# Performance work log

Hardware: AMD Instinct MI355X
Metric: run time of the kernel (lower is better)

## Reference

```python
import jax, jax.numpy as jnp
import numpy as np

N, D = 512, 128


def setup_inputs() -> dict:
    key = jax.random.key(0)
    k1, k2 = jax.random.split(key)
    source = jax.random.normal(k1, (N, D), dtype=jnp.float32)
    target = jax.random.normal(k2, (N, D), dtype=jnp.float32)
    return {"source": source, "target": target}


def _distance_matrix(x):
    # pairwise squared-euclidean distances, same broadcast form as torch source
    return jnp.sum((x[:, None, :] - x[None, :, :]) ** 2, axis=-1)  # [n,n]


def reference(source, target):
    n = source.shape[0]
    C_s = _distance_matrix(source)  # [n,n]
    C_t = _distance_matrix(target)  # [n,n]
    # cost[i,j,k] = |C_s[i,j] - C_t[i,k]|  -> [n,n,n]
    cost = jnp.abs(C_s[:, :, None] - C_t[:, None, :])
    # transport_plan = outer(1/n, 1/n) is constant uniform 1/n^2;
    # the torch loop recomputes the identical value max_iter times, so one pass suffices.
    plan = jnp.float32(1.0) / (n * n)
    gw_dist = jnp.sum(cost * cost) * plan
    return gw_dist
```

## Files before the change

kernel.cpp:

```cpp
#include <hip/hip_runtime.h>

#define N 512
#define D 128


__device__ __forceinline__ float wave_reduce_add_f32(float v) {
    #pragma unroll
    for (int off = 32; off > 0; off >>= 1)
        v += __shfl_down(v, off, 64);
    return v;
}

__global__ __launch_bounds__(256) void gw_dist(
    const float* __restrict__ src, const float* __restrict__ tgt,
    double* __restrict__ rs, double* __restrict__ ss)
{
    __shared__ float tile[32 * 257];
    __shared__ float redf[4][8];

    const int b  = blockIdx.x;
    const int m  = b >> 8;
    const int iq = (b >> 1) & 127;
    const int jh = b & 1;
    const int t  = threadIdx.x;
    const int i0 = iq * 4;
    const int j0 = jh * 256;

    const float*  X  = m ? tgt : src;
    const float4* X4 = reinterpret_cast<const float4*>(X + j0 * D);

    const int jhome = t >> 3;
    const int d4    = t & 7;

    float a0 = 0.f, a1 = 0.f, a2 = 0.f, a3 = 0.f;

    for (int c = 0; c < 4; ++c) {
        if (c) __syncthreads();

        #pragma unroll
        for (int p = 0; p < 8; ++p) {
            int jr = p * 32 + jhome;
            float4 v = X4[jr * 32 + c * 8 + d4];
            tile[(d4 * 4 + 0) * 257 + jr] = v.x;
            tile[(d4 * 4 + 1) * 257 + jr] = v.y;
            tile[(d4 * 4 + 2) * 257 + jr] = v.z;
            tile[(d4 * 4 + 3) * 257 + jr] = v.w;
        }
        __syncthreads();

        const int dbase = c * 32;
        const float* r0 = X + (i0 + 0) * D + dbase;
        const float* r1 = X + (i0 + 1) * D + dbase;
        const float* r2 = X + (i0 + 2) * D + dbase;
        const float* r3 = X + (i0 + 3) * D + dbase;

        #pragma unroll
        for (int dd = 0; dd < 32; ++dd) {
            float v = tile[dd * 257 + t];
            float e;
            e = r0[dd] - v; a0 += e * e;
            e = r1[dd] - v; a1 += e * e;
            e = r2[dd] - v; a2 += e * e;
            e = r3[dd] - v; a3 += e * e;
        }
    }

    float qv[8];
    qv[0] = a0; qv[1] = a1; qv[2] = a2; qv[3] = a3;
    qv[4] = a0 * a0; qv[5] = a1 * a1; qv[6] = a2 * a2; qv[7] = a3 * a3;

    const int wave = t >> 6;
    const int lane = t & 63;
    #pragma unroll
    for (int k = 0; k < 8; ++k) {
        float v = wave_reduce_add_f32(qv[k]);
        if (lane == 0) redf[wave][k] = v;
    }
    __syncthreads();

    if (t == 0) {
        const int base = ((jh << 1) | m) * N + i0;
        #pragma unroll
        for (int k = 0; k < 4; ++k) {
            double rsk = (double)redf[0][k]     + (double)redf[1][k]
                       + (double)redf[2][k]     + (double)redf[3][k];
            double ssk = (double)redf[0][k + 4] + (double)redf[1][k + 4]
                       + (double)redf[2][k + 4] + (double)redf[3][k + 4];
            rs[base + k] = rsk;
            ss[base + k] = ssk;
        }
    }
}

__global__ __launch_bounds__(512) void gw_finalize(
    const double* __restrict__ rs, const double* __restrict__ ss,
    float* __restrict__ out)
{
    const int i = threadIdx.x;

    const double rs_s = rs[0 * N + i] + rs[2 * N + i];
    const double rs_t = rs[1 * N + i] + rs[3 * N + i];
    const double ss_s = ss[0 * N + i] + ss[2 * N + i];
    const double ss_t = ss[1 * N + i] + ss[3 * N + i];

    double v = (double)N * (ss_s + ss_t) - 2.0 * rs_s * rs_t;
    #pragma unroll
    for (int off = 32; off > 0; off >>= 1)
        v += __shfl_down(v, off, 64);

    __shared__ double sm[8];
    const int wave = i >> 6;
    const int lane = i & 63;
    if (lane == 0) sm[wave] = v;
    __syncthreads();

    if (i == 0) {
        double total = 0.0;
        #pragma unroll
        for (int w = 0; w < 8; ++w) total += sm[w];
        out[0] = (float)(total / ((double)N * (double)N));
    }
}

extern "C" void kernel_launch(void* const* d_in, const int* in_sizes, int n_in,
                              void* d_out, int out_size, void* d_ws, size_t ws_size,
                              hipStream_t stream) {
    const float* src = (const float*)d_in[0];
    const float* tgt = (const float*)d_in[1];
    float* out = (float*)d_out;

    double* rs = (double*)d_ws;
    double* ss = rs + 4 * N;

    gw_dist    <<<dim3(512), dim3(256), 0, stream>>>(src, tgt, rs, ss);
    gw_finalize<<<dim3(1),   dim3(512), 0, stream>>>(rs, ss, out);
}
```

Baseline: 16.25 us.

## Prefetch next chunk into registers and use XOR-swizzled float4 shared layout

The column tile is now stored as swizzled float4 rows instead of a transposed scalar tile with padding, so the inner loop reads one vectorized LDS load per four dimensions. The next chunk's global loads are issued into registers right after the barrier, so they overlap the compute on the current chunk. This raises register pressure (eight extra float4s per thread) and moves the barrier to the end of the loop.

```diff
diff --git a/kernel.cpp b/kernel.cpp
--- a/kernel.cpp
+++ b/kernel.cpp
@@ -4,19 +4,12 @@
 #define D 128
 
 
-__device__ __forceinline__ float wave_reduce_add_f32(float v) {
-    #pragma unroll
-    for (int off = 32; off > 0; off >>= 1)
-        v += __shfl_down(v, off, 64);
-    return v;
-}
-
 __global__ __launch_bounds__(256) void gw_dist(
     const float* __restrict__ src, const float* __restrict__ tgt,
     double* __restrict__ rs, double* __restrict__ ss)
 {
-    __shared__ float tile[32 * 257];
-    __shared__ float redf[4][8];
+    __shared__ float4 buf[256 * 8];
+    __shared__ float  redf[4][8];
 
     const int b  = blockIdx.x;
     const int m  = b >> 8;
@@ -29,24 +22,29 @@
     const float*  X  = m ? tgt : src;
     const float4* X4 = reinterpret_cast<const float4*>(X + j0 * D);
 
-    const int jhome = t >> 3;
-    const int d4    = t & 7;
+    const int jr0 = t >> 3;
+    const int s   = t & 7;
 
     float a0 = 0.f, a1 = 0.f, a2 = 0.f, a3 = 0.f;
+    float4 pre[8];
+
+    #pragma unroll
+    for (int p = 0; p < 8; ++p)
+        pre[p] = X4[(p * 32 + jr0) * 32 + s];
 
     for (int c = 0; c < 4; ++c) {
-        if (c) __syncthreads();
-
         #pragma unroll
         for (int p = 0; p < 8; ++p) {
-            int jr = p * 32 + jhome;
-            float4 v = X4[jr * 32 + c * 8 + d4];
-            tile[(d4 * 4 + 0) * 257 + jr] = v.x;
-            tile[(d4 * 4 + 1) * 257 + jr] = v.y;
-            tile[(d4 * 4 + 2) * 257 + jr] = v.z;
-            tile[(d4 * 4 + 3) * 257 + jr] = v.w;
+            int jr = p * 32 + jr0;
+            buf[jr * 8 + (s ^ (jr & 7))] = pre[p];
         }
         __syncthreads();
+
+        if (c < 3) {
+            #pragma unroll
+            for (int p = 0; p < 8; ++p)
+                pre[p] = X4[(p * 32 + jr0) * 32 + (c + 1) * 8 + s];
+        }
 
         const int dbase = c * 32;
         const float* r0 = X + (i0 + 0) * D + dbase;
@@ -55,14 +53,28 @@
         const float* r3 = X + (i0 + 3) * D + dbase;
 
         #pragma unroll
-        for (int dd = 0; dd < 32; ++dd) {
-            float v = tile[dd * 257 + t];
+        for (int sl = 0; sl < 8; ++sl) {
+            float4 v = buf[t * 8 + (sl ^ (t & 7))];
             float e;
-            e = r0[dd] - v; a0 += e * e;
-            e = r1[dd] - v; a1 += e * e;
-            e = r2[dd] - v; a2 += e * e;
-            e = r3[dd] - v; a3 += e * e;
+            e = r0[4 * sl + 0] - v.x; a0 += e * e;
+            e = r1[4 * sl + 0] - v.x; a1 += e * e;
+            e = r2[4 * sl + 0] - v.x; a2 += e * e;
+            e = r3[4 * sl + 0] - v.x; a3 += e * e;
+            e = r0[4 * sl + 1] - v.y; a0 += e * e;
+            e = r1[4 * sl + 1] - v.y; a1 += e * e;
+            e = r2[4 * sl + 1] - v.y; a2 += e * e;
+            e = r3[4 * sl + 1] - v.y; a3 += e * e;
+            e = r0[4 * sl + 2] - v.z; a0 += e * e;
+            e = r1[4 * sl + 2] - v.z; a1 += e * e;
+            e = r2[4 * sl + 2] - v.z; a2 += e * e;
+            e = r3[4 * sl + 2] - v.z; a3 += e * e;
+            e = r0[4 * sl + 3] - v.w; a0 += e * e;
+            e = r1[4 * sl + 3] - v.w; a1 += e * e;
+            e = r2[4 * sl + 3] - v.w; a2 += e * e;
+            e = r3[4 * sl + 3] - v.w; a3 += e * e;
         }
+
+        if (c < 3) __syncthreads();
     }
 
     float qv[8];
@@ -73,7 +85,10 @@
     const int lane = t & 63;
     #pragma unroll
     for (int k = 0; k < 8; ++k) {
-        float v = wave_reduce_add_f32(qv[k]);
+        float v = qv[k];
+        #pragma unroll
+        for (int off = 32; off > 0; off >>= 1)
+            v += __shfl_down(v, off, 64);
         if (lane == 0) redf[wave][k] = v;
     }
     __syncthreads();
```

After: 30.91 us. 1.9x slower.
